# Kernel optimization log

Hardware: AMD Instinct MI355X
Metric: run time of the kernel (lower is better)

Reference implementation:

```python
import jax, jax.numpy as jnp
import numpy as np

# Reference for Net.get_seed_aff_x4 (+ Sinkhorn), the custom-kernel hotspot of this
# module. The ResNet50 conv stack / side convs are standard cuDNN-covered ops and the
# external `resnet50` module is not part of this source; `feature` here is hie_fea
# (768ch at side3 resolution) and `norm_cam` is the bg-augmented CAM at the same
# resolution, exactly as they arrive at get_seed_aff_x4 in forward.

N, C, H, W, CF = 8, 21, 64, 64, 768
NUM_CLUSTERS = 2
KMEANS_ITERS = 10      # deterministic Lloyd iterations (external kmeans_pytorch is
                       # randomly initialized; we use first-two-valid-pixel init)
EPS_OT = 0.1
SINK_MAX_ITER = 100
SINK_THRESH = 0.01


def setup_inputs() -> dict:
    key = jax.random.key(0)
    k1, k2, k3 = jax.random.split(key, 3)
    norm_cam = jax.random.uniform(k1, (N, C, H, W), dtype=jnp.float32)
    label = (jax.random.uniform(k2, (N, C, 1, 1)) < 0.8).astype(jnp.float32)
    label = label.at[:, 0].set(1.0)  # background always present
    feature = jax.random.normal(k3, (N, CF, H, W), dtype=jnp.float32)
    return {"norm_cam": norm_cam, "label": label, "feature": feature}


def _kmeans_cosine(feat, feat_n, mask):
    # feat: [HW, CF] raw features, feat_n: [HW, CF] l2-normalized, mask: [HW] in {0,1}
    valid = mask > 0
    cnt = valid.sum()
    order = jnp.argsort(jnp.where(valid, 0, 1))  # stable: valid pixels first
    init = feat[order[:NUM_CLUSTERS]] * mask[order[:NUM_CLUSTERS], None]

    def step(centers, _):
        cn = centers / jnp.maximum(
            jnp.linalg.norm(centers, axis=-1, keepdims=True), 1e-8)
        sim = feat_n @ cn.T                                  # [HW, K]
        assign = jnp.argmax(sim, axis=-1)
        oh = jax.nn.one_hot(assign, NUM_CLUSTERS, dtype=feat.dtype) * mask[:, None]
        counts = oh.sum(0)
        new_c = (oh.T @ feat) / jnp.maximum(counts, 1.0)[:, None]
        return new_c, None

    centers, _ = jax.lax.scan(step, init, None, length=KMEANS_ITERS)
    # original `continue` when < num_clusters valid pixels -> centers stay zero
    return jnp.where(cnt >= NUM_CLUSTERS, centers, jnp.zeros_like(centers))


def _sinkhorn(K, u, v):
    # K: [C, M, Nk]; faithful to Net.Sinkhorn incl. early stop on mean |r - r0|
    def cond(state):
        i, r, c, err = state
        return (i < SINK_MAX_ITER) & (err >= SINK_THRESH)

    def body(state):
        i, r, c, _ = state
        r0 = r
        r = u / jnp.einsum('cmk,ck->cm', K, c)
        c = v / jnp.einsum('cmk,cm->ck', K, r)
        err = jnp.abs(r - r0).mean()
        return (i + 1, r, c, err)

    state0 = (jnp.int32(0), jnp.ones_like(u), jnp.ones_like(v),
              jnp.asarray(jnp.inf, u.dtype))
    _, r, c, _ = jax.lax.while_loop(cond, body, state0)
    return r[..., None] * c[..., None, :] * K


def reference(norm_cam, label, feature):
    n, c, h, w = norm_cam.shape
    cf = feature.shape[1]
    hw = h * w

    # seeds: one-hot argmax of norm_cam, gated by image-level labels
    belonging = jnp.argmax(norm_cam, axis=1)                       # [n,h,w]
    seeds = jnp.transpose(jax.nn.one_hot(belonging, c, dtype=norm_cam.dtype),
                          (0, 3, 1, 2)) * label                    # [n,c,h,w]
    # nearest-interp to feature size is identity (same HxW by construction)
    mask = seeds.reshape(n, c, hw)                                 # [n,c,hw]

    feat = feature.reshape(n, cf, hw).transpose(0, 2, 1)           # [n,hw,cf]
    feat_n = feat / jnp.maximum(
        jnp.linalg.norm(feat, axis=-1, keepdims=True), 1e-8)

    # per-(image, class) cosine k-means, fully vectorized (no python data loops)
    centers = jax.vmap(
        lambda f, fn, ms: jax.vmap(_kmeans_cosine, in_axes=(None, None, 0))(f, fn, ms)
    )(feat, feat_n, mask)                                          # [n,c,K,cf]
    cnt = (mask > 0).sum(-1)                                       # [n,c]

    # cosine similarity of ALL pixels to the 2 centers, mean over clusters
    centers_n = centers / jnp.maximum(
        jnp.linalg.norm(centers, axis=-1, keepdims=True), 1e-8)
    cos = jnp.einsum('nmd,nckd->nckm', feat_n, centers_n)          # [n,c,K,hw]
    cam = jnp.where((cnt >= NUM_CLUSTERS)[..., None],
                    cos.mean(axis=2), 0.0).reshape(n, c, h, w)

    # --- Sinkhorn OT refinement (torch.no_grad in original) ---
    feat_ot = feat / (jnp.linalg.norm(feat, axis=-1, keepdims=True) + 1e-5)
    cflat = centers.reshape(n, c * NUM_CLUSTERS, cf)
    cflat = cflat / (jnp.linalg.norm(cflat, axis=-1, keepdims=True) + 1e-5)
    sim = jnp.einsum('nmd,njd->nmj', feat_ot, cflat)               # [n,hw,c*K]
    # faithful to original's sim.view(M, N, n_cls).permute(2, 0, 1)
    sim = sim.reshape(n, hw, NUM_CLUSTERS, c).transpose(0, 3, 1, 2)  # [n,c,hw,K]
    Kmat = jax.lax.stop_gradient(jnp.exp(-(1.0 - sim) / EPS_OT))
    u = jnp.full((c, hw), 1.0 / hw, dtype=sim.dtype)
    v = jnp.full((c, NUM_CLUSTERS), 1.0 / NUM_CLUSTERS, dtype=sim.dtype)
    T = jax.vmap(lambda Kb: _sinkhorn(Kb, u, v))(Kmat)             # [n,c,hw,K]
    T = T.transpose(0, 1, 3, 2).reshape(n, c, NUM_CLUSTERS, h, w)

    # all_cam_maps.mean(dim=2) * label, then per-map max normalization
    out = cam * label
    out = out / (out.max(axis=(2, 3), keepdims=True) + 1e-5)
    return out, T


if __name__ == '__main__':
    o = reference(**setup_inputs())
    print(o[0].shape, o[1].shape)
```

## Files before the change

kernel.cpp:

```cpp
#include <hip/hip_runtime.h>
#include <hip/hip_bf16.h>
#include <stdint.h>

#define NIMG 8
#define NCLS 21
#define HW   4096
#define CF   768
#define NK   2
#define NJ   42
#define NJP  48
#define SINK_MAX 100

using uint32 = unsigned int;
using u16    = unsigned short;

__device__ __forceinline__ float b2f(u16 u){ union{uint32 i; float f;} x; x.i=((uint32)u)<<16; return x.f; }
__device__ __forceinline__ u16 f2b(float f){ union{float f; uint32 i;} x; x.f=f; return (u16)((x.i + 0x7fffu + ((x.i>>16)&1u))>>16); }

template<int BF>
__device__ __forceinline__ float ldin(const void* p, size_t idx){
    if (BF) return b2f(((const u16*)p)[idx]);
    return ((const float*)p)[idx];
}
template<int BF>
__device__ __forceinline__ void stout(void* p, size_t idx, float v){
    if (BF) ((u16*)p)[idx] = f2b(v);
    else    ((float*)p)[idx] = v;
}

__global__ void k_detect(const void* feat, int* flag){
    __shared__ int cnt;
    if (threadIdx.x == 0) cnt = 0;
    __syncthreads();
    const u16* f = (const u16*)feat;
    int bad = 0;
    for (int i = threadIdx.x; i < 4096; i += 256){
        int ex = (f[i] >> 7) & 0xFF;
        if (ex >= 160) bad++;
    }
    atomicAdd(&cnt, bad);
    __syncthreads();
    if (threadIdx.x == 0) *flag = (cnt < 64) ? 1 : 0;
}

template<int BF>
__global__ void k_seeds(const void* __restrict__ cam, const void* __restrict__ label,
                        int* __restrict__ pix_cls, const int* __restrict__ dflag){
    if (*dflag != BF) return;
    int g = blockIdx.x*256 + threadIdx.x;
    int n = g >> 12, p = g & 4095;
    float best = -1e30f; int bel = 0;
    for (int c = 0; c < NCLS; c++){
        float v = ldin<BF>(cam, (size_t)(n*NCLS + c)*HW + p);
        if (v > best){ best = v; bel = c; }
    }
    pix_cls[g] = (ldin<BF>(label, n*NCLS + bel) > 0.f) ? bel : -1;
}

template<int BF>
__global__ void k_norms(const void* __restrict__ feat, float* __restrict__ inv_n,
                        float* __restrict__ inv_ot, const int* __restrict__ dflag){
    if (*dflag != BF) return;
    int g = blockIdx.x*256 + threadIdx.x;
    int n = g >> 12, p = g & 4095;
    double s = 0.0;
    for (int k = 0; k < CF; k++){
        double v = (double)ldin<BF>(feat, (size_t)(n*CF + k)*HW + p);
        s += v*v;
    }
    double nr = sqrt(s);
    inv_n [g] = (float)(1.0/fmax(nr, 1e-8));
    inv_ot[g] = (float)(1.0/(nr + 1e-5));
}

template<int BF>
__global__ void k_transpose(const void* __restrict__ feat, float* __restrict__ featT,
                            const int* __restrict__ dflag){
    if (*dflag != BF) return;
    __shared__ float tile[64][65];
    int b = blockIdx.x;
    int n   = b / ((CF/64)*(HW/64));
    int rem = b % ((CF/64)*(HW/64));
    int kb = (rem / (HW/64)) * 64;
    int pb = (rem % (HW/64)) * 64;
    int tx = threadIdx.x & 63, ty = threadIdx.x >> 6;
    for (int i = 0; i < 16; i++){
        int k = ty*16 + i;
        tile[tx][k] = ldin<BF>(feat, ((size_t)(n*CF + kb + k))*HW + pb + tx);
    }
    __syncthreads();
    for (int i = 0; i < 16; i++){
        int p = ty*16 + i;
        featT[((size_t)(n*HW + pb + p))*CF + kb + tx] = tile[p][tx];
    }
}

__global__ void k_scan(const int* __restrict__ pix_cls, const float* __restrict__ featT,
                       int* __restrict__ cnt, int* __restrict__ plist,
                       double* __restrict__ centers){
    int b = blockIdx.x; int n = b / NCLS, c = b % NCLS;
    int lane = threadIdx.x;
    int* lst = plist + (size_t)b*HW;
    int count = 0, i0 = -1, i1 = -1;
    for (int base = 0; base < HW; base += 64){
        int cls = pix_cls[n*HW + base + lane];
        unsigned long long m = __ballot(cls == c);
        int pos = count + __popcll(m & ((1ull<<lane) - 1ull));
        if (cls == c) lst[pos] = base + lane;
        if (i0 < 0){
            if (m){ i0 = base + __ffsll((long long)m) - 1;
                    unsigned long long m2 = m & (m-1);
                    if (m2) i1 = base + __ffsll((long long)m2) - 1; }
        } else if (i1 < 0){
            if (m) i1 = base + __ffsll((long long)m) - 1;
        }
        count += __popcll(m);
    }
    if (lane == 0) cnt[b] = count;
    double* C0 = centers + (size_t)b*NK*CF;
    if (count >= 2){
        const float* r0 = featT + (size_t)(n*HW + i0)*CF;
        const float* r1 = featT + (size_t)(n*HW + i1)*CF;
        for (int e = lane; e < CF; e += 64){ C0[e] = (double)r0[e]; C0[CF+e] = (double)r1[e]; }
    } else {
        for (int e = lane; e < CF; e += 64){ C0[e] = 0.0; C0[CF+e] = 0.0; }
    }
}

__global__ __launch_bounds__(512) void k_kmeans(const int* __restrict__ cnt,
                                                const int* __restrict__ plist,
                                                const float* __restrict__ featT,
                                                double* __restrict__ centers){
    int b = blockIdx.x; int n = b / NCLS;
    int m = cnt[b];
    if (m < 2) return;
    __shared__ double Cs[2][CF];
    __shared__ float  As[2][CF];
    __shared__ double red[2];
    __shared__ float  ck[2];
    __shared__ double invn[2];
    __shared__ unsigned char asg[HW];
    __shared__ int chg;
    int tid = threadIdx.x, lane = tid & 63, w = tid >> 6;
    const int* lst = plist + (size_t)b*HW;
    double* Cg = centers + (size_t)b*NK*CF;
    for (int j = tid; j < CF; j += 512){ Cs[0][j] = Cg[j]; Cs[1][j] = Cg[CF+j]; }
    for (int i = tid; i < m; i += 512) asg[i] = 255;
    __syncthreads();
    for (int it = 0; it < 10; it++){
        if (tid < 2){ red[tid] = 0.0; ck[tid] = 0.f; }
        if (tid == 0) chg = 0;
        __syncthreads();
        double q0 = 0.0, q1 = 0.0;
        for (int j = tid; j < CF; j += 512){ q0 += Cs[0][j]*Cs[0][j]; q1 += Cs[1][j]*Cs[1][j]; }
        #pragma unroll
        for (int off = 32; off; off >>= 1){ q0 += __shfl_xor(q0, off); q1 += __shfl_xor(q1, off); }
        if (lane == 0){ atomicAdd(&red[0], q0); atomicAdd(&red[1], q1); }
        for (int j = tid; j < CF; j += 512){ As[0][j] = 0.f; As[1][j] = 0.f; }
        __syncthreads();
        if (tid == 0){
            invn[0] = 1.0/fmax(sqrt(red[0]), 1e-8);
            invn[1] = 1.0/fmax(sqrt(red[1]), 1e-8);
        }
        __syncthreads();
        double ic0 = invn[0], ic1 = invn[1];
        double c0r[12], c1r[12];
        #pragma unroll
        for (int s = 0; s < 3; s++){
            #pragma unroll
            for (int t = 0; t < 4; t++){
                int e = lane*4 + s*256 + t;
                c0r[s*4+t] = Cs[0][e];
                c1r[s*4+t] = Cs[1][e];
            }
        }
        float a0[12], a1[12];
        #pragma unroll
        for (int j = 0; j < 12; j++){ a0[j] = 0.f; a1[j] = 0.f; }
        int c0n = 0, c1n = 0, myChg = 0;
        float vA[4][12], vB[4][12];
        if (w < m){
            #pragma unroll
            for (int p = 0; p < 4; p++){
                int idx = w + 8*p; int iv = (idx < m) ? idx : (m-1);
                const float* row = featT + (size_t)(n*HW + lst[iv])*CF + lane*4;
                *(float4*)&vA[p][0] = *(const float4*)(row);
                *(float4*)&vA[p][4] = *(const float4*)(row + 256);
                *(float4*)&vA[p][8] = *(const float4*)(row + 512);
            }
        }
        for (int i = w; i < m; i += 32){
            int inext = i + 32;
            if (inext < m){
                #pragma unroll
                for (int p = 0; p < 4; p++){
                    int idx = inext + 8*p; int iv = (idx < m) ? idx : (m-1);
                    const float* row = featT + (size_t)(n*HW + lst[iv])*CF + lane*4;
                    *(float4*)&vB[p][0] = *(const float4*)(row);
                    *(float4*)&vB[p][4] = *(const float4*)(row + 256);
                    *(float4*)&vB[p][8] = *(const float4*)(row + 512);
                }
            }
            double d0[4], d1[4];
            #pragma unroll
            for (int p = 0; p < 4; p++){
                double s0 = 0.0, s1 = 0.0;
                #pragma unroll
                for (int j = 0; j < 12; j++){
                    s0 += (double)vA[p][j]*c0r[j];
                    s1 += (double)vA[p][j]*c1r[j];
                }
                d0[p] = s0; d1[p] = s1;
            }
            #pragma unroll
            for (int off = 32; off; off >>= 1){
                #pragma unroll
                for (int p = 0; p < 4; p++){
                    d0[p] += __shfl_xor(d0[p], off);
                    d1[p] += __shfl_xor(d1[p], off);
                }
            }
            #pragma unroll
            for (int p = 0; p < 4; p++){
                int idx = i + 8*p;
                if (idx < m){
                    int a = (d0[p]*ic0 >= d1[p]*ic1) ? 0 : 1;
                    if (lane == 0){
                        if (asg[idx] != (unsigned char)a){ myChg++; asg[idx] = (unsigned char)a; }
                    }
                    if (a == 0){ c0n++;
                        #pragma unroll
                        for (int j = 0; j < 12; j++) a0[j] += vA[p][j];
                    } else { c1n++;
                        #pragma unroll
                        for (int j = 0; j < 12; j++) a1[j] += vA[p][j];
                    }
                }
            }
            #pragma unroll
            for (int p = 0; p < 4; p++){
                #pragma unroll
                for (int j = 0; j < 12; j++) vA[p][j] = vB[p][j];
            }
        }
        #pragma unroll
        for (int s = 0; s < 3; s++){
            #pragma unroll
            for (int t = 0; t < 4; t++){
                int e = lane*4 + s*256 + t;
                atomicAdd(&As[0][e], a0[s*4+t]);
                atomicAdd(&As[1][e], a1[s*4+t]);
            }
        }
        if (lane == 0){
            atomicAdd(&ck[0], (float)c0n); atomicAdd(&ck[1], (float)c1n);
            if (myChg) atomicAdd(&chg, myChg);
        }
        __syncthreads();
        if (chg == 0) break;
        double dv0 = fmax((double)ck[0], 1.0), dv1 = fmax((double)ck[1], 1.0);
        for (int j = tid; j < CF; j += 512){
            Cs[0][j] = (double)As[0][j]/dv0; Cs[1][j] = (double)As[1][j]/dv1;
        }
        __syncthreads();
    }
    for (int j = tid; j < CF; j += 512){ Cg[j] = Cs[0][j]; Cg[CF+j] = Cs[1][j]; }
}

__global__ void k_invc(const double* __restrict__ centers, float* __restrict__ invc_cam,
                       float* __restrict__ invc_ot){
    int b = blockIdx.x;
    int lane = threadIdx.x;
    const double* C = centers + (size_t)b*CF;
    double s = 0.0;
    for (int e = lane; e < CF; e += 64) s += C[e]*C[e];
    for (int off = 32; off; off >>= 1) s += __shfl_xor(s, off);
    if (lane == 0){
        double nr = sqrt(s);
        invc_cam[b] = (float)(1.0/fmax(nr, 1e-8));
        invc_ot[b]  = (float)(1.0/(nr + 1e-5));
    }
}

__global__ void k_cf32(const double* __restrict__ centers, float* __restrict__ Cf32){
    int n = blockIdx.x; int tid = threadIdx.x;
    for (int idx = tid; idx < NJP*CF; idx += 256){
        int j = idx / CF, e = idx - j*CF;
        float v = (j < NJ) ? (float)centers[((size_t)n*NJ + j)*CF + e] : 0.f;
        Cf32[(size_t)n*NJP*CF + idx] = v;
    }
}

__global__ __launch_bounds__(256) void k_gemmf(const float* __restrict__ featT,
                                               const float* __restrict__ Cf32,
                                               float* __restrict__ D){
    __shared__ float Fs[128][66];
    int b = blockIdx.x; int n = b >> 6; int pbase = (b & 63)*64;
    int tid = threadIdx.x, p = tid & 63;
    int jb = __builtin_amdgcn_readfirstlane((tid >> 6)*12);
    float acc[12];
    #pragma unroll
    for (int j = 0; j < 12; j++) acc[j] = 0.f;
    for (int kc = 0; kc < CF; kc += 128){
        __syncthreads();
        for (int idx = tid; idx < 64*64; idx += 256){
            int pp = idx >> 6, cw = idx & 63;
            float2 wv = *(const float2*)(featT + (size_t)(n*HW + pbase + pp)*CF + kc + cw*2);
            Fs[cw*2    ][pp] = wv.x;
            Fs[cw*2 + 1][pp] = wv.y;
        }
        __syncthreads();
        const float* Cb = Cf32 + (size_t)n*NJP*CF + kc;
        for (int k8 = 0; k8 < 128; k8 += 8){
            #pragma unroll
            for (int j = 0; j < 12; j++){
                const float* cr = Cb + (size_t)(jb + j)*CF + k8;
                #pragma unroll
                for (int k = 0; k < 8; k++)
                    acc[j] += Fs[k8 + k][p] * cr[k];
            }
        }
    }
    float* dp = D + ((size_t)(n*HW + pbase + p))*NJP + jb;
    #pragma unroll
    for (int j = 0; j < 12; j++) dp[j] = acc[j];
}

template<int BF>
__global__ __launch_bounds__(256) void k_out0(const float* __restrict__ D,
                                              const float* __restrict__ inv_n,
                                              const float* __restrict__ invc_cam,
                                              const int* __restrict__ cnt,
                                              void* __restrict__ out0,
                                              const int* __restrict__ dflag){
    if (*dflag != BF) return;
    int b = blockIdx.x; int n = b / NCLS, c = b % NCLS;
    __shared__ float wmax[4]; __shared__ float sden;
    int tid = threadIdx.x, lane = tid & 63, w = tid >> 6;
    size_t obase = (size_t)b*HW;
    if (cnt[b] < 2){
        for (int p = tid; p < HW; p += 256) stout<BF>(out0, obase + p, 0.f);
        return;
    }
    float ic0 = invc_cam[n*NJ + 2*c], ic1 = invc_cam[n*NJ + 2*c + 1];
    const float* Dn = D + (size_t)n*HW*NJP;
    float mx = -1e30f;
    for (int p = tid; p < HW; p += 256){
        const float* dp = Dn + (size_t)p*NJP + 2*c;
        float camv = 0.5f*(dp[0]*ic0 + dp[1]*ic1)*inv_n[n*HW + p];
        mx = fmaxf(mx, camv);
    }
    for (int off = 32; off; off >>= 1) mx = fmaxf(mx, __shfl_xor(mx, off));
    if (lane == 0) wmax[w] = mx;
    __syncthreads();
    if (tid == 0) sden = fmaxf(fmaxf(wmax[0], wmax[1]), fmaxf(wmax[2], wmax[3])) + 1e-5f;
    __syncthreads();
    float den = sden;
    for (int p = tid; p < HW; p += 256){
        const float* dp = Dn + (size_t)p*NJP + 2*c;
        float camv = 0.5f*(dp[0]*ic0 + dp[1]*ic1)*inv_n[n*HW + p];
        stout<BF>(out0, obase + p, camv/den);
    }
}

__global__ void k_kmat(const float* __restrict__ D, const float* __restrict__ inv_ot,
                       const float* __restrict__ invc_ot, float* __restrict__ Kg,
                       float* __restrict__ errg, int* __restrict__ arrv){
    if (blockIdx.x == 0){
        for (int i = threadIdx.x; i < NIMG*(SINK_MAX+1); i += 256){ errg[i] = 0.f; arrv[i] = 0; }
    }
    int g = blockIdx.x*256 + threadIdx.x;
    int n = g / (NCLS*HW);
    int rem = g - n*(NCLS*HW);
    int c = rem >> 12, p = rem & 4095;
    const float* dp = D + ((size_t)n*HW + p)*NJP;
    float io = inv_ot[n*HW + p];
    float s0 = dp[c]      * io * invc_ot[n*NJ + c];
    float s1 = dp[21 + c] * io * invc_ot[n*NJ + 21 + c];
    Kg[(size_t)g*2 + 0] = expf((s0 - 1.f)*10.f);
    Kg[(size_t)g*2 + 1] = expf((s1 - 1.f)*10.f);
}

template<int BF>
__global__ __launch_bounds__(256) void k_sink(const float* __restrict__ Kg,
                                              float* __restrict__ errg,
                                              int* __restrict__ arrv,
                                              void* __restrict__ d_out,
                                              const int* __restrict__ dflag){
    if (*dflag != BF) return;
    __shared__ float K0s[HW]; __shared__ float K1s[HW]; __shared__ float rs[HW];
    __shared__ float wred[4][3]; __shared__ float sh[3];
    int b = blockIdx.x; int n = b / NCLS;
    int tid = threadIdx.x, lane = tid & 63, w = tid >> 6;
    const float* Kb = Kg + (size_t)b*HW*2;
    for (int p = tid; p < HW; p += 256){ K0s[p] = Kb[p*2]; K1s[p] = Kb[p*2+1]; rs[p] = 1.f; }
    float cc0 = 1.f, cc1 = 1.f, err = 1e30f;
    const float u = 1.f/4096.f;
    int iter = 0;
    __syncthreads();
    while (iter < SINK_MAX && err >= 0.01f){
        float p0 = 0.f, p1 = 0.f, es = 0.f;
        for (int p = tid; p < HW; p += 256){
            float k0 = K0s[p], k1 = K1s[p];
            float rn = u / (k0*cc0 + k1*cc1);
            es += fabsf(rn - rs[p]);
            rs[p] = rn;
            p0 += k0*rn; p1 += k1*rn;
        }
        #pragma unroll
        for (int off = 32; off; off >>= 1){
            p0 += __shfl_xor(p0, off); p1 += __shfl_xor(p1, off); es += __shfl_xor(es, off);
        }
        if (lane == 0){ wred[w][0] = p0; wred[w][1] = p1; wred[w][2] = es; }
        __syncthreads();
        if (tid == 0){
            float P0 = wred[0][0]+wred[1][0]+wred[2][0]+wred[3][0];
            float P1 = wred[0][1]+wred[1][1]+wred[2][1]+wred[3][1];
            float ES = wred[0][2]+wred[1][2]+wred[2][2]+wred[3][2];
            sh[0] = 0.5f/P0; sh[1] = 0.5f/P1;
            int slot = n*(SINK_MAX+1) + iter;
            atomicAdd(&errg[slot], ES);
            __threadfence();
            atomicAdd(&arrv[slot], 1);
            while (__hip_atomic_load(&arrv[slot], __ATOMIC_ACQUIRE, __HIP_MEMORY_SCOPE_AGENT) < NCLS)
                __builtin_amdgcn_s_sleep(8);
            sh[2] = __hip_atomic_load(&errg[slot], __ATOMIC_RELAXED, __HIP_MEMORY_SCOPE_AGENT)
                    * (1.f/((float)NCLS*HW));
        }
        __syncthreads();
        cc0 = sh[0]; cc1 = sh[1]; err = sh[2];
        iter++;
    }
    size_t o1 = (size_t)NIMG*NCLS*HW + (size_t)b*NK*HW;
    for (int p = tid; p < HW; p += 256){
        float rv = rs[p];
        stout<BF>(d_out, o1 + p,      rv*cc0*K0s[p]);
        stout<BF>(d_out, o1 + HW + p, rv*cc1*K1s[p]);
    }
}

extern "C" void kernel_launch(void* const* d_in, const int* in_sizes, int n_in,
                              void* d_out, int out_size, void* d_ws, size_t ws_size,
                              hipStream_t stream){
    const void* cam   = d_in[0];
    const void* label = d_in[1];
    const void* feat  = d_in[2];

    char* ws = (char*)d_ws; size_t off = 0;
    auto alloc = [&](size_t bytes)->char*{
        char* p = ws + off; off = (off + bytes + 255) & ~(size_t)255; return p;
    };
    int*    dflag    = (int*)   alloc(4);
    float*  featT    = (float*) alloc((size_t)NIMG*HW*CF*4);
    double* centers  = (double*)alloc((size_t)NIMG*NCLS*NK*CF*8);
    float*  Cf32     = (float*) alloc((size_t)NIMG*NJP*CF*4);
    float*  inv_n    = (float*) alloc((size_t)NIMG*HW*4);
    float*  inv_ot   = (float*) alloc((size_t)NIMG*HW*4);
    int*    pix_cls  = (int*)   alloc((size_t)NIMG*HW*4);
    int*    cnt      = (int*)   alloc((size_t)NIMG*NCLS*4);
    int*    plist    = (int*)   alloc((size_t)NIMG*NCLS*HW*4);
    float*  invc_cam = (float*) alloc((size_t)NIMG*NJ*4);
    float*  invc_ot  = (float*) alloc((size_t)NIMG*NJ*4);
    float*  D        = (float*) alloc((size_t)NIMG*HW*NJP*4);
    float*  Kg       = (float*) alloc((size_t)NIMG*NCLS*HW*NK*4);
    float*  errg     = (float*) alloc((size_t)NIMG*(SINK_MAX+1)*4);
    int*    arrv     = (int*)   alloc((size_t)NIMG*(SINK_MAX+1)*4);

    k_detect<<<1, 256, 0, stream>>>(feat, dflag);

    k_seeds<1><<<NIMG*HW/256, 256, 0, stream>>>(cam, label, pix_cls, dflag);
    k_seeds<0><<<NIMG*HW/256, 256, 0, stream>>>(cam, label, pix_cls, dflag);
    k_norms<1><<<NIMG*HW/256, 256, 0, stream>>>(feat, inv_n, inv_ot, dflag);
    k_norms<0><<<NIMG*HW/256, 256, 0, stream>>>(feat, inv_n, inv_ot, dflag);
    k_transpose<1><<<NIMG*(CF/64)*(HW/64), 256, 0, stream>>>(feat, featT, dflag);
    k_transpose<0><<<NIMG*(CF/64)*(HW/64), 256, 0, stream>>>(feat, featT, dflag);

    k_scan  <<<NIMG*NCLS, 64, 0, stream>>>(pix_cls, featT, cnt, plist, centers);
    k_kmeans<<<NIMG*NCLS, 512, 0, stream>>>(cnt, plist, featT, centers);
    k_invc  <<<NIMG*NJ, 64, 0, stream>>>(centers, invc_cam, invc_ot);
    k_cf32  <<<NIMG, 256, 0, stream>>>(centers, Cf32);
    k_gemmf <<<NIMG*64, 256, 0, stream>>>(featT, Cf32, D);

    k_out0<1><<<NIMG*NCLS, 256, 0, stream>>>(D, inv_n, invc_cam, cnt, d_out, dflag);
    k_out0<0><<<NIMG*NCLS, 256, 0, stream>>>(D, inv_n, invc_cam, cnt, d_out, dflag);

    k_kmat  <<<NIMG*NCLS*HW/256, 256, 0, stream>>>(D, inv_ot, invc_ot, Kg, errg, arrv);

    k_sink<1><<<NIMG*NCLS, 256, 0, stream>>>(Kg, errg, arrv, d_out, dflag);
    k_sink<0><<<NIMG*NCLS, 256, 0, stream>>>(Kg, errg, arrv, d_out, dflag);
}
```

Baseline: 671.4 us.

## Restructure k-means: 16-lane pixel groups, derive cluster-1 sums from totals

Each wavefront now handles four pixels concurrently, using 16 lanes per pixel with 48 features per lane. This replaces full-wave shuffle reductions with four ds_swizzle steps on doubles. A one-time per-class total feature sum is precomputed, so only cluster-0 sums are accumulated and cluster-1 is derived as total minus cluster-0. This halves accumulator registers and LDS atomics. Centers are staged in a padded LDS layout and the pixel list is cached in LDS. The cost is more registers per thread (48-wide vA/vB/a0 arrays) under launch_bounds(512,2), and the subtraction-derived centroid introduces small float rounding differences.

Result: slower. 1.254 ms (+86.8%).

```diff
diff --git a/kernel.cpp b/kernel.cpp
--- a/kernel.cpp
+++ b/kernel.cpp
@@ -26,6 +26,15 @@
 __device__ __forceinline__ void stout(void* p, size_t idx, float v){
     if (BF) ((u16*)p)[idx] = f2b(v);
     else    ((float*)p)[idx] = v;
+}
+
+template<int IMM>
+__device__ __forceinline__ double swz_add_f64(double v){
+    union{ double d; unsigned int u[2]; } x, y;
+    x.d = v;
+    y.u[0] = __builtin_amdgcn_ds_swizzle(x.u[0], IMM);
+    y.u[1] = __builtin_amdgcn_ds_swizzle(x.u[1], IMM);
+    return v + y.d;
 }
 
 __global__ void k_detect(const void* feat, int* flag){
@@ -127,36 +136,70 @@
     }
 }
 
-__global__ __launch_bounds__(512) void k_kmeans(const int* __restrict__ cnt,
-                                                const int* __restrict__ plist,
-                                                const float* __restrict__ featT,
-                                                double* __restrict__ centers){
+__global__ __launch_bounds__(512, 2) void k_kmeans(const int* __restrict__ cnt,
+                                                   const int* __restrict__ plist,
+                                                   const float* __restrict__ featT,
+                                                   double* __restrict__ centers){
     int b = blockIdx.x; int n = b / NCLS;
     int m = cnt[b];
     if (m < 2) return;
     __shared__ double Cs[2][CF];
-    __shared__ float  As[2][CF];
+    __shared__ double Cs2[2][16][49];
+    __shared__ float  As[CF];
+    __shared__ float  St[CF];
     __shared__ double red[2];
-    __shared__ float  ck[2];
+    __shared__ float  ck0;
     __shared__ double invn[2];
     __shared__ unsigned char asg[HW];
+    __shared__ int    lst_s[HW];
     __shared__ int chg;
     int tid = threadIdx.x, lane = tid & 63, w = tid >> 6;
+    int sl = lane & 15;
+    int g  = lane >> 4;
     const int* lst = plist + (size_t)b*HW;
     double* Cg = centers + (size_t)b*NK*CF;
-    for (int j = tid; j < CF; j += 512){ Cs[0][j] = Cg[j]; Cs[1][j] = Cg[CF+j]; }
-    for (int i = tid; i < m; i += 512) asg[i] = 255;
-    __syncthreads();
+    for (int j = tid; j < CF; j += 512){ Cs[0][j] = Cg[j]; Cs[1][j] = Cg[CF+j]; St[j] = 0.f; }
+    for (int i = tid; i < m; i += 512){ asg[i] = 255; lst_s[i] = lst[i]; }
+    __syncthreads();
+
+    {
+        float a0[48];
+        #pragma unroll
+        for (int j = 0; j < 48; j++) a0[j] = 0.f;
+        for (int i = w; i < m; i += 32){
+            int idx = i + 8*g;
+            if (idx < m){
+                const float* row = featT + (size_t)(n*HW + lst_s[idx])*CF + 4*sl;
+                float vv[48];
+                #pragma unroll
+                for (int t = 0; t < 12; t++) *(float4*)&vv[t*4] = *(const float4*)(row + t*64);
+                #pragma unroll
+                for (int j = 0; j < 48; j++) a0[j] += vv[j];
+            }
+        }
+        #pragma unroll
+        for (int j = 0; j < 48; j++){
+            int e = 4*sl + 64*(j>>2) + (j&3);
+            atomicAdd(&St[e], a0[j]);
+        }
+    }
+    __syncthreads();
+
     for (int it = 0; it < 10; it++){
-        if (tid < 2){ red[tid] = 0.0; ck[tid] = 0.f; }
-        if (tid == 0) chg = 0;
+        if (tid < 2) red[tid] = 0.0;
+        if (tid == 0){ ck0 = 0.f; chg = 0; }
         __syncthreads();
         double q0 = 0.0, q1 = 0.0;
         for (int j = tid; j < CF; j += 512){ q0 += Cs[0][j]*Cs[0][j]; q1 += Cs[1][j]*Cs[1][j]; }
         #pragma unroll
         for (int off = 32; off; off >>= 1){ q0 += __shfl_xor(q0, off); q1 += __shfl_xor(q1, off); }
         if (lane == 0){ atomicAdd(&red[0], q0); atomicAdd(&red[1], q1); }
-        for (int j = tid; j < CF; j += 512){ As[0][j] = 0.f; As[1][j] = 0.f; }
+        for (int j = tid; j < CF; j += 512) As[j] = 0.f;
+        for (int e = tid; e < CF; e += 512){
+            int u = e & 3, s = (e >> 2) & 15, t = e >> 6;
+            Cs2[0][s][t*4 + u] = Cs[0][e];
+            Cs2[1][s][t*4 + u] = Cs[1][e];
+        }
         __syncthreads();
         if (tid == 0){
             invn[0] = 1.0/fmax(sqrt(red[0]), 1e-8);
@@ -164,103 +207,84 @@
         }
         __syncthreads();
         double ic0 = invn[0], ic1 = invn[1];
-        double c0r[12], c1r[12];
+        const double* c0row = Cs2[0][sl];
+        const double* c1row = Cs2[1][sl];
+        float a0[48];
         #pragma unroll
-        for (int s = 0; s < 3; s++){
+        for (int j = 0; j < 48; j++) a0[j] = 0.f;
+        int c0n = 0, c1n = 0, myChg = 0;
+        float vA[48], vB[48];
+        if (w < m){
+            int idx = w + 8*g; int iv = (idx < m) ? idx : (m-1);
+            const float* row = featT + (size_t)(n*HW + lst_s[iv])*CF + 4*sl;
             #pragma unroll
-            for (int t = 0; t < 4; t++){
-                int e = lane*4 + s*256 + t;
-                c0r[s*4+t] = Cs[0][e];
-                c1r[s*4+t] = Cs[1][e];
-            }
-        }
-        float a0[12], a1[12];
-        #pragma unroll
-        for (int j = 0; j < 12; j++){ a0[j] = 0.f; a1[j] = 0.f; }
-        int c0n = 0, c1n = 0, myChg = 0;
-        float vA[4][12], vB[4][12];
-        if (w < m){
+            for (int t = 0; t < 12; t++) *(float4*)&vA[t*4] = *(const float4*)(row + t*64);
+        }
+        if (w + 32 < m){
+            int idx = w + 32 + 8*g; int iv = (idx < m) ? idx : (m-1);
+            const float* row = featT + (size_t)(n*HW + lst_s[iv])*CF + 4*sl;
             #pragma unroll
-            for (int p = 0; p < 4; p++){
-                int idx = w + 8*p; int iv = (idx < m) ? idx : (m-1);
-                const float* row = featT + (size_t)(n*HW + lst[iv])*CF + lane*4;
-                *(float4*)&vA[p][0] = *(const float4*)(row);
-                *(float4*)&vA[p][4] = *(const float4*)(row + 256);
-                *(float4*)&vA[p][8] = *(const float4*)(row + 512);
-            }
+            for (int t = 0; t < 12; t++) *(float4*)&vB[t*4] = *(const float4*)(row + t*64);
         }
         for (int i = w; i < m; i += 32){
-            int inext = i + 32;
-            if (inext < m){
-                #pragma unroll
-                for (int p = 0; p < 4; p++){
-                    int idx = inext + 8*p; int iv = (idx < m) ? idx : (m-1);
-                    const float* row = featT + (size_t)(n*HW + lst[iv])*CF + lane*4;
-                    *(float4*)&vB[p][0] = *(const float4*)(row);
-                    *(float4*)&vB[p][4] = *(const float4*)(row + 256);
-                    *(float4*)&vB[p][8] = *(const float4*)(row + 512);
-                }
-            }
-            double d0[4], d1[4];
+            double s0a = 0.0, s0b = 0.0, s1a = 0.0, s1b = 0.0;
             #pragma unroll
-            for (int p = 0; p < 4; p++){
-                double s0 = 0.0, s1 = 0.0;
-                #pragma unroll
-                for (int j = 0; j < 12; j++){
-                    s0 += (double)vA[p][j]*c0r[j];
-                    s1 += (double)vA[p][j]*c1r[j];
-                }
-                d0[p] = s0; d1[p] = s1;
+            for (int j = 0; j < 24; j++){
+                double fv = (double)vA[j];
+                s0a += fv * c0row[j];
+                s1a += fv * c1row[j];
             }
             #pragma unroll
-            for (int off = 32; off; off >>= 1){
-                #pragma unroll
-                for (int p = 0; p < 4; p++){
-                    d0[p] += __shfl_xor(d0[p], off);
-                    d1[p] += __shfl_xor(d1[p], off);
+            for (int j = 24; j < 48; j++){
+                double fv = (double)vA[j];
+                s0b += fv * c0row[j];
+                s1b += fv * c1row[j];
+            }
+            double d0 = s0a + s0b, d1 = s1a + s1b;
+            d0 = swz_add_f64<0x201F>(d0); d1 = swz_add_f64<0x201F>(d1);
+            d0 = swz_add_f64<0x101F>(d0); d1 = swz_add_f64<0x101F>(d1);
+            d0 = swz_add_f64<0x081F>(d0); d1 = swz_add_f64<0x081F>(d1);
+            d0 = swz_add_f64<0x041F>(d0); d1 = swz_add_f64<0x041F>(d1);
+            int idx = i + 8*g;
+            if (idx < m){
+                int a = (d0*ic0 >= d1*ic1) ? 0 : 1;
+                if (sl == 0){
+                    if (asg[idx] != (unsigned char)a){ myChg++; asg[idx] = (unsigned char)a; }
+                    if (a == 0) c0n++; else c1n++;
+                }
+                if (a == 0){
+                    #pragma unroll
+                    for (int j = 0; j < 48; j++) a0[j] += vA[j];
                 }
             }
             #pragma unroll
-            for (int p = 0; p < 4; p++){
-                int idx = i + 8*p;
-                if (idx < m){
-                    int a = (d0[p]*ic0 >= d1[p]*ic1) ? 0 : 1;
-                    if (lane == 0){
-                        if (asg[idx] != (unsigned char)a){ myChg++; asg[idx] = (unsigned char)a; }
-                    }
-                    if (a == 0){ c0n++;
-                        #pragma unroll
-                        for (int j = 0; j < 12; j++) a0[j] += vA[p][j];
-                    } else { c1n++;
-                        #pragma unroll
-                        for (int j = 0; j < 12; j++) a1[j] += vA[p][j];
-                    }
-                }
+            for (int j = 0; j < 48; j++) vA[j] = vB[j];
+            int inext = i + 64;
+            if (inext < m){
+                int idx2 = inext + 8*g; int iv2 = (idx2 < m) ? idx2 : (m-1);
+                const float* row = featT + (size_t)(n*HW + lst_s[iv2])*CF + 4*sl;
+                #pragma unroll
+                for (int t = 0; t < 12; t++) *(float4*)&vB[t*4] = *(const float4*)(row + t*64);
             }
-            #pragma unroll
-            for (int p = 0; p < 4; p++){
-                #pragma unroll
-                for (int j = 0; j < 12; j++) vA[p][j] = vB[p][j];
-            }
         }
         #pragma unroll
-        for (int s = 0; s < 3; s++){
-            #pragma unroll
-            for (int t = 0; t < 4; t++){
-                int e = lane*4 + s*256 + t;
-                atomicAdd(&As[0][e], a0[s*4+t]);
-                atomicAdd(&As[1][e], a1[s*4+t]);
-            }
-        }
-        if (lane == 0){
-            atomicAdd(&ck[0], (float)c0n); atomicAdd(&ck[1], (float)c1n);
+        for (int j = 0; j < 48; j++){
+            int e = 4*sl + 64*(j>>2) + (j&3);
+            atomicAdd(&As[e], a0[j]);
+        }
+        if (sl == 0){
+            atomicAdd(&ck0, (float)c0n);
             if (myChg) atomicAdd(&chg, myChg);
         }
+        (void)c1n;
         __syncthreads();
         if (chg == 0) break;
-        double dv0 = fmax((double)ck[0], 1.0), dv1 = fmax((double)ck[1], 1.0);
+        double dv0 = fmax((double)ck0, 1.0);
+        double dv1 = fmax((double)((float)m - ck0), 1.0);
         for (int j = tid; j < CF; j += 512){
-            Cs[0][j] = (double)As[0][j]/dv0; Cs[1][j] = (double)As[1][j]/dv1;
+            float A0 = As[j];
+            Cs[0][j] = (double)A0/dv0;
+            Cs[1][j] = (double)(St[j] - A0)/dv1;
         }
         __syncthreads();
     }
```
